# Kernel optimization log

Measured on AMD Instinct MI355X. Metric: run time of the kernel, lower is better.

The kernel has to match this reference:

```python
import jax, jax.numpy as jnp
import numpy as np

LN_EPS = 1e-5


def setup_inputs() -> dict:
    key = jax.random.key(0)
    kx, kA, kB, kC, kg = jax.random.split(key, 5)
    B, S, D, N = 16, 1024, 1024, 64
    x = jax.random.uniform(kx, (B, S, D), dtype=jnp.float32)
    A = jax.random.uniform(kA, (D, N), dtype=jnp.float32)          # torch.rand init
    W_B = jax.random.normal(kB, (N, D), dtype=jnp.float32) * 0.02  # B: d_model -> d_state
    W_C = jax.random.normal(kC, (D, N), dtype=jnp.float32) * 0.02  # C.weight_raw, [d_model, d_state]
    gamma = jax.random.normal(kg, (D,), dtype=jnp.float32) * 0.1   # TopologicalNorm scale (sigmoid-bounded)
    return {"x": x, "A": A, "W_B": W_B, "W_C": W_C, "gamma": gamma}


def reference(x, A, W_B, W_C, gamma):
    # x: [B, S, D]
    Bb, S, D = x.shape
    N = A.shape[1]
    A_sig = jax.nn.sigmoid(A)          # [D, N] state decay gates
    Bw = jax.nn.sigmoid(W_B)           # [N, D] sigmoid-constrained input projection
    Cw = jax.nn.sigmoid(W_C)           # [D, N] sigmoid-constrained readout weights
    g = jax.nn.sigmoid(gamma)          # [D]   bounded norm scale

    def step(h, x_t):
        # x_t: [B, D], h: [B, D, N]
        b_t = x_t @ Bw.T                                             # [B, N]
        inp = b_t[:, None, :] * x_t[:, :, None]                      # [B, D, N] outer product morphism
        h = jnp.clip(h * A_sig[None] + inp, 0.0, 1.0)                # clamped state update
        y = jnp.sum(h * Cw[None], axis=-1)                           # [B, D] weighted readout
        mu = jnp.mean(y, axis=-1, keepdims=True)
        var = jnp.var(y, axis=-1, keepdims=True)
        y = (y - mu) * jax.lax.rsqrt(var + LN_EPS) * g               # TopologicalNorm
        return h, y

    h0 = jnp.zeros((Bb, D, N), dtype=x.dtype)
    _, ys = jax.lax.scan(step, h0, jnp.swapaxes(x, 0, 1))            # ys: [S, B, D]
    y = jnp.swapaxes(ys, 0, 1)                                       # [B, S, D]
    return jnp.clip(y + x, 0.0, 1.0)
```

## Files before the change

kernel.cpp:

```cpp
#include <hip/hip_runtime.h>
#include <math.h>

#define D_MODEL 1024
#define N_STATE 64
#define BATCH   16
#define SEQ     1024
#define CS      16
#define SEGLEN  512
#define WARM    64
#define SAT_T   1.0001f
#define LPS     20

__device__ __forceinline__ float sigmoidf_dev(float v) {
    return 1.0f / (1.0f + expf(-v));
}

template<int CTRL>
__device__ __forceinline__ float dpp_add(float v) {
    int s = __builtin_amdgcn_update_dpp(0, __float_as_int(v), CTRL, 0xF, 0xF, true);
    return v + __int_as_float(s);
}

template<int CTRL>
__device__ __forceinline__ float dpp_min(float v) {
    int s = __builtin_amdgcn_update_dpp(0, __float_as_int(v), CTRL, 0xF, 0xF, true);
    return fminf(v, __int_as_float(s));
}

#define CLAMP01(v) __builtin_amdgcn_fmed3f((v), 0.0f, 1.0f)

__global__ __launch_bounds__(256) void k0_precompute(
        const float* __restrict__ A, const float* __restrict__ W_B,
        const float* __restrict__ W_C, const float* __restrict__ gamma,
        float* __restrict__ A_sig, float* __restrict__ BwT,
        float* __restrict__ Cs, float* __restrict__ gs) {
    int i = blockIdx.x * 256 + threadIdx.x;
    if (i < D_MODEL * N_STATE) {
        A_sig[i] = sigmoidf_dev(A[i]);
        Cs[i]    = sigmoidf_dev(W_C[i]);
        int d = i >> 6, n = i & 63;
        BwT[i] = sigmoidf_dev(W_B[n * D_MODEL + d]);
        if (i < D_MODEL) gs[i] = sigmoidf_dev(gamma[i]);
    }
}

__global__ __launch_bounds__(256) void k0b_csum(
        const float* __restrict__ Cs, float* __restrict__ csum) {
    int d = blockIdx.x * 256 + threadIdx.x;
    if (d >= D_MODEL) return;
    const float4* c = (const float4*)(Cs + (size_t)d * N_STATE);
    float w[16];
#pragma unroll
    for (int q = 0; q < 16; ++q) {
        float4 v = c[q];
        w[q] = (v.x + v.y) + (v.z + v.w);
    }
#pragma unroll
    for (int off = 1; off < 16; off <<= 1) {
        float tmp[16];
#pragma unroll
        for (int q = 0; q < 16; ++q) tmp[q] = w[q] + w[q ^ off];
#pragma unroll
        for (int q = 0; q < 16; ++q) w[q] = tmp[q];
    }
    csum[d] = w[0];
}

__global__ __launch_bounds__(256) void k1_bt_gemm(
        const float* __restrict__ x, const float* __restrict__ BwT,
        float* __restrict__ bt, float* __restrict__ btmin) {
    __shared__ float xs[2][32][17];
    __shared__ float bs[2][32][64];

    const int t  = threadIdx.x;
    const int r  = t >> 4;
    const int c  = t & 15;
    const int m0 = blockIdx.x * 16;

    const int xr = t >> 4;
    const int xk = (t & 15) * 2;

    float acc[4] = {0.f, 0.f, 0.f, 0.f};

    {
        float2 xv = *(const float2*)(x + (size_t)(m0 + xr) * D_MODEL + xk);
        float4 b0 = *(const float4*)(BwT + t * 4);
        float4 b1 = *(const float4*)(BwT + 1024 + t * 4);
        xs[0][xk + 0][xr] = xv.x;
        xs[0][xk + 1][xr] = xv.y;
        *(float4*)(&bs[0][0][0] + t * 4)        = b0;
        *(float4*)(&bs[0][0][0] + 1024 + t * 4) = b1;
    }
    __syncthreads();

    for (int kc = 0; kc < 32; ++kc) {
        const int p = kc & 1;
        float2 xv; float4 b0, b1;
        const bool more = (kc + 1 < 32);
        if (more) {
            const int k0 = (kc + 1) * 32;
            xv = *(const float2*)(x + (size_t)(m0 + xr) * D_MODEL + k0 + xk);
            b0 = *(const float4*)(BwT + (size_t)k0 * N_STATE + t * 4);
            b1 = *(const float4*)(BwT + (size_t)k0 * N_STATE + 1024 + t * 4);
        }
#pragma unroll
        for (int kk = 0; kk < 32; ++kk) {
            float  a  = xs[p][kk][r];
            float4 bq = *(const float4*)(&bs[p][kk][c * 4]);
            acc[0] = fmaf(a, bq.x, acc[0]);
            acc[1] = fmaf(a, bq.y, acc[1]);
            acc[2] = fmaf(a, bq.z, acc[2]);
            acc[3] = fmaf(a, bq.w, acc[3]);
        }
        if (more) {
            const int q = 1 - p;
            xs[q][xk + 0][xr] = xv.x;
            xs[q][xk + 1][xr] = xv.y;
            *(float4*)(&bs[q][0][0] + t * 4)        = b0;
            *(float4*)(&bs[q][0][0] + 1024 + t * 4) = b1;
        }
        __syncthreads();
    }

    *(float4*)(&bt[(size_t)(m0 + r) * N_STATE + c * 4]) =
        make_float4(acc[0], acc[1], acc[2], acc[3]);

    float bm = fminf(fminf(acc[0], acc[1]), fminf(acc[2], acc[3]));
    bm = dpp_min<0xB1>(bm); bm = dpp_min<0x4E>(bm);
    bm = dpp_min<0x141>(bm); bm = dpp_min<0x140>(bm);
    if (c == 0) btmin[m0 + r] = bm;
}

__global__ __launch_bounds__(256, 8) void k2_scan(
        const float* __restrict__ x, const float* __restrict__ bt,
        const float* __restrict__ btmin,
        const float* __restrict__ A_sig, const float* __restrict__ Cs,
        float* __restrict__ y_raw) {
    const int t    = threadIdx.x;
    const int lane = t & 63;
    const int wv   = t >> 6;
    const int nq   = lane & 15;
    const int cl   = wv * 4 + (lane >> 4);
    const int bid  = blockIdx.x;
    const int seg  = bid & 1;
    const int dg   = (bid >> 1) & 63;
    const int b    = bid >> 7;
    const int d0   = dg * 16;
    const int d    = d0 + cl;

    const int nWarm  = seg ? (WARM / CS) : 0;
    const int nTot   = nWarm + (SEGLEN / CS);
    const int sStart = seg * SEGLEN - nWarm * CS;

    __shared__ __align__(16) float lbt [2][CS * 64];
    __shared__ __align__(16) float lx  [2][CS * 16];
    __shared__ __align__(16) float lpxT[2][16 * LPS];

    const float4 av = *(const float4*)(A_sig + (size_t)d * N_STATE + nq * 4);
    const float4 cv = *(const float4*)(Cs    + (size_t)d * N_STATE + nq * 4);

    float h0 = 0.f, h1 = 0.f, h2 = 0.f, h3 = 0.f;

    const float* btp  = bt    + (size_t)b * SEQ * N_STATE + (size_t)sStart * N_STATE;
    const float* btmp = btmin + (size_t)b * SEQ + sStart;
    const float* xpp  = x + (size_t)b * SEQ * D_MODEL + (size_t)sStart * D_MODEL + d0;
    float* ystore = y_raw + (size_t)b * SEQ * D_MODEL + (size_t)seg * SEGLEN * D_MODEL + d;

    const int xst = t >> 4;
    const int xdd = t & 15;

    {
        float4 b4 = *(const float4*)(btp + t * 4);
        float  xv = xpp[(size_t)xst * D_MODEL + xdd];
        float  bm = fmaxf(btmp[xst], 0.f);
        *(float4*)(&lbt[0][t * 4]) = b4;
        lx[0][t] = xv;
        lpxT[0][xdd * LPS + xst] = xv * bm;
    }
    btp  += CS * N_STATE;
    btmp += CS;
    xpp  += (size_t)CS * D_MODEL;
    __syncthreads();

    for (int ch = 0; ch < nTot; ++ch) {
        const int p = ch & 1;
        float4 nb; float nx, npx;
        const bool more = (ch + 1 < nTot);
        if (more) {
            nb  = *(const float4*)(btp + t * 4);
            nx  = xpp[(size_t)xst * D_MODEL + xdd];
            npx = nx * fmaxf(btmp[xst], 0.f);
            btp  += CS * N_STATE;
            btmp += CS;
            xpp  += (size_t)CS * D_MODEL;
        }

        const float* Lb = lbt[p];
        const float* Lx = lx [p];
        const float* Lp = &lpxT[p][cl * LPS];

        if (ch < nWarm) {
#pragma unroll
            for (int g = 0; g < 4; ++g) {
                const float4 pq = *(const float4*)(Lp + g * 4);
                const float qmin = fminf(fminf(pq.x, pq.y), fminf(pq.z, pq.w));
                if (__all(qmin >= SAT_T)) { h0 = h1 = h2 = h3 = 1.f; continue; }
                const float pmv[4] = {pq.x, pq.y, pq.z, pq.w};
#pragma unroll
                for (int j = 0; j < 4; ++j) {
                    const int i = g * 4 + j;
                    const float pm = pmv[j];
                    if (__all(pm >= SAT_T)) { h0 = h1 = h2 = h3 = 1.f; continue; }
                    const float  xt = Lx[i * 16 + cl];
                    const float4 bv = *(const float4*)(Lb + i * 64 + nq * 4);
                    h0 = CLAMP01(fmaf(h0, av.x, bv.x * xt));
                    h1 = CLAMP01(fmaf(h1, av.y, bv.y * xt));
                    h2 = CLAMP01(fmaf(h2, av.z, bv.z * xt));
                    h3 = CLAMP01(fmaf(h3, av.w, bv.w * xt));
                }
            }
        } else {
#pragma unroll
            for (int g = 0; g < 4; ++g) {
                const float4 pq = *(const float4*)(Lp + g * 4);
                const float qmin = fminf(fminf(pq.x, pq.y), fminf(pq.z, pq.w));
                if (__all(qmin >= SAT_T)) { h0 = h1 = h2 = h3 = 1.f; continue; }
                const float pmv[4] = {pq.x, pq.y, pq.z, pq.w};
#pragma unroll
                for (int j = 0; j < 4; ++j) {
                    const int i = g * 4 + j;
                    const float pm = pmv[j];
                    if (__all(pm >= SAT_T)) { h0 = h1 = h2 = h3 = 1.f; continue; }
                    const float  xt = Lx[i * 16 + cl];
                    const float4 bv = *(const float4*)(Lb + i * 64 + nq * 4);
                    h0 = CLAMP01(fmaf(h0, av.x, bv.x * xt));
                    h1 = CLAMP01(fmaf(h1, av.y, bv.y * xt));
                    h2 = CLAMP01(fmaf(h2, av.z, bv.z * xt));
                    h3 = CLAMP01(fmaf(h3, av.w, bv.w * xt));
                    float y = fmaf(h0, cv.x, h1 * cv.y) + fmaf(h2, cv.z, h3 * cv.w);
                    y = dpp_add<0xB1>(y);
                    y = dpp_add<0x4E>(y);
                    y = dpp_add<0x141>(y);
                    y = dpp_add<0x140>(y);
                    if (nq == 0 && !(pm >= SAT_T)) ystore[(size_t)i * D_MODEL] = y;
                }
            }
            ystore += (size_t)CS * D_MODEL;
        }

        if (more) {
            const int q = 1 - p;
            *(float4*)(&lbt[q][t * 4]) = nb;
            lx[q][t] = nx;
            lpxT[q][xdd * LPS + xst] = npx;
        }
        __syncthreads();
    }
}

__global__ __launch_bounds__(256, 1) void k3_norm(
        const float* __restrict__ x, const float* __restrict__ gs,
        const float* __restrict__ btmin, const float* __restrict__ csum,
        float* __restrict__ y) {
    const int row = blockIdx.x;
    const int t   = threadIdx.x;
    const size_t base = (size_t)row * D_MODEL + t * 4;
    const float bm = fmaxf(btmin[row], 0.f);

    float4 xv  = *(const float4*)(x + base);
    float4 cs4 = *(const float4*)(csum + t * 4);
    const bool p0 = (xv.x * bm >= SAT_T);
    const bool p1 = (xv.y * bm >= SAT_T);
    const bool p2 = (xv.z * bm >= SAT_T);
    const bool p3 = (xv.w * bm >= SAT_T);
    float y0 = cs4.x, y1 = cs4.y, y2 = cs4.z, y3 = cs4.w;
    if (!(p0 && p1 && p2 && p3)) {
        float4 ld = *(const float4*)(y + base);
        if (!p0) y0 = ld.x;
        if (!p1) y1 = ld.y;
        if (!p2) y2 = ld.z;
        if (!p3) y3 = ld.w;
    }

    float s1 = (y0 + y1) + (y2 + y3);
#pragma unroll
    for (int off = 32; off > 0; off >>= 1) s1 += __shfl_xor(s1, off);

    __shared__ float red[8];
    const int w = t >> 6;
    if ((t & 63) == 0) red[w] = s1;
    __syncthreads();
    const float mu = (red[0] + red[1] + red[2] + red[3]) * (1.0f / (float)D_MODEL);

    const float dx0 = y0 - mu, dx1 = y1 - mu, dx2 = y2 - mu, dx3 = y3 - mu;
    float s2 = (dx0 * dx0 + dx1 * dx1) + (dx2 * dx2 + dx3 * dx3);
#pragma unroll
    for (int off = 32; off > 0; off >>= 1) s2 += __shfl_xor(s2, off);
    if ((t & 63) == 0) red[4 + w] = s2;
    __syncthreads();
    const float var = (red[4] + red[5] + red[6] + red[7]) * (1.0f / (float)D_MODEL);
    const float rs  = 1.0f / sqrtf(var + 1e-5f);

    float4 gv = *(const float4*)(gs + t * 4);
    float4 o;
    o.x = fminf(fmaxf(dx0 * rs * gv.x + xv.x, 0.f), 1.f);
    o.y = fminf(fmaxf(dx1 * rs * gv.y + xv.y, 0.f), 1.f);
    o.z = fminf(fmaxf(dx2 * rs * gv.z + xv.z, 0.f), 1.f);
    o.w = fminf(fmaxf(dx3 * rs * gv.w + xv.w, 0.f), 1.f);
    *(float4*)(y + base) = o;
}

extern "C" void kernel_launch(void* const* d_in, const int* in_sizes, int n_in,
                              void* d_out, int out_size, void* d_ws, size_t ws_size,
                              hipStream_t stream) {
    (void)in_sizes; (void)n_in; (void)out_size; (void)ws_size;
    const float* x     = (const float*)d_in[0];
    const float* A     = (const float*)d_in[1];
    const float* W_B   = (const float*)d_in[2];
    const float* W_C   = (const float*)d_in[3];
    const float* gamma = (const float*)d_in[4];
    float* out = (float*)d_out;
    float* ws  = (float*)d_ws;

    float* bt    = ws;
    float* A_sig = ws + 1048576;
    float* BwT   = ws + 1048576 + 65536;
    float* Cs    = ws + 1048576 + 2 * 65536;
    float* gs    = ws + 1048576 + 3 * 65536;
    float* btmin = ws + 1048576 + 3 * 65536 + 1024;
    float* csum  = ws + 1048576 + 3 * 65536 + 1024 + 16384;

    k0_precompute<<<dim3(256), dim3(256), 0, stream>>>(A, W_B, W_C, gamma,
                                                       A_sig, BwT, Cs, gs);
    k0b_csum<<<dim3(4), dim3(256), 0, stream>>>(Cs, csum);
    k1_bt_gemm<<<dim3(1024), dim3(256), 0, stream>>>(x, BwT, bt, btmin);
    k2_scan<<<dim3(2048), dim3(256), 0, stream>>>(x, bt, btmin, A_sig, Cs, out);
    k3_norm<<<dim3(BATCH * SEQ), dim3(256), 0, stream>>>(x, gs, btmin, csum, out);
}
```

Measured before the change: 231.8 us.

## Retile bt GEMM to 32 rows per block, load B weights directly into registers

Measured after the change: 259.2 us. 1.12x slower.

```diff
diff --git a/kernel.cpp b/kernel.cpp
--- a/kernel.cpp
+++ b/kernel.cpp
@@ -69,66 +69,79 @@
 __global__ __launch_bounds__(256) void k1_bt_gemm(
         const float* __restrict__ x, const float* __restrict__ BwT,
         float* __restrict__ bt, float* __restrict__ btmin) {
-    __shared__ float xs[2][32][17];
-    __shared__ float bs[2][32][64];
+    __shared__ float xs[2][16][36];
 
     const int t  = threadIdx.x;
     const int r  = t >> 4;
     const int c  = t & 15;
-    const int m0 = blockIdx.x * 16;
-
-    const int xr = t >> 4;
-    const int xk = (t & 15) * 2;
-
-    float acc[4] = {0.f, 0.f, 0.f, 0.f};
+    const int m0 = blockIdx.x * 32;
+
+    const int sm = t >> 3;
+    const int sk = (t & 7) * 2;
+
+    float acc[2][4];
+#pragma unroll
+    for (int i = 0; i < 2; ++i)
+#pragma unroll
+        for (int j = 0; j < 4; ++j) acc[i][j] = 0.0f;
 
     {
-        float2 xv = *(const float2*)(x + (size_t)(m0 + xr) * D_MODEL + xk);
-        float4 b0 = *(const float4*)(BwT + t * 4);
-        float4 b1 = *(const float4*)(BwT + 1024 + t * 4);
-        xs[0][xk + 0][xr] = xv.x;
-        xs[0][xk + 1][xr] = xv.y;
-        *(float4*)(&bs[0][0][0] + t * 4)        = b0;
-        *(float4*)(&bs[0][0][0] + 1024 + t * 4) = b1;
+        float2 xv = *(const float2*)(x + (size_t)(m0 + sm) * D_MODEL + sk);
+        xs[0][sk + 0][sm] = xv.x;
+        xs[0][sk + 1][sm] = xv.y;
     }
     __syncthreads();
 
-    for (int kc = 0; kc < 32; ++kc) {
-        const int p = kc & 1;
-        float2 xv; float4 b0, b1;
-        const bool more = (kc + 1 < 32);
-        if (more) {
-            const int k0 = (kc + 1) * 32;
-            xv = *(const float2*)(x + (size_t)(m0 + xr) * D_MODEL + k0 + xk);
-            b0 = *(const float4*)(BwT + (size_t)k0 * N_STATE + t * 4);
-            b1 = *(const float4*)(BwT + (size_t)k0 * N_STATE + 1024 + t * 4);
-        }
-#pragma unroll
-        for (int kk = 0; kk < 32; ++kk) {
-            float  a  = xs[p][kk][r];
-            float4 bq = *(const float4*)(&bs[p][kk][c * 4]);
-            acc[0] = fmaf(a, bq.x, acc[0]);
-            acc[1] = fmaf(a, bq.y, acc[1]);
-            acc[2] = fmaf(a, bq.z, acc[2]);
-            acc[3] = fmaf(a, bq.w, acc[3]);
-        }
+    for (int kt = 0; kt < 64; ++kt) {
+        const int p = kt & 1;
+        const bool more = (kt + 1 < 64);
+
+        float4 breg[16];
+#pragma unroll
+        for (int kk = 0; kk < 16; ++kk)
+            breg[kk] = *(const float4*)(BwT + (size_t)(kt * 16 + kk) * N_STATE + c * 4);
+
+        float2 xv;
+        if (more)
+            xv = *(const float2*)(x + (size_t)(m0 + sm) * D_MODEL + (kt + 1) * 16 + sk);
+
+#pragma unroll
+        for (int kk = 0; kk < 16; ++kk) {
+            float2 ap = *(const float2*)(&xs[p][kk][r * 2]);
+            acc[0][0] = fmaf(ap.x, breg[kk].x, acc[0][0]);
+            acc[0][1] = fmaf(ap.x, breg[kk].y, acc[0][1]);
+            acc[0][2] = fmaf(ap.x, breg[kk].z, acc[0][2]);
+            acc[0][3] = fmaf(ap.x, breg[kk].w, acc[0][3]);
+            acc[1][0] = fmaf(ap.y, breg[kk].x, acc[1][0]);
+            acc[1][1] = fmaf(ap.y, breg[kk].y, acc[1][1]);
+            acc[1][2] = fmaf(ap.y, breg[kk].z, acc[1][2]);
+            acc[1][3] = fmaf(ap.y, breg[kk].w, acc[1][3]);
+        }
+
         if (more) {
             const int q = 1 - p;
-            xs[q][xk + 0][xr] = xv.x;
-            xs[q][xk + 1][xr] = xv.y;
-            *(float4*)(&bs[q][0][0] + t * 4)        = b0;
-            *(float4*)(&bs[q][0][0] + 1024 + t * 4) = b1;
+            xs[q][sk + 0][sm] = xv.x;
+            xs[q][sk + 1][sm] = xv.y;
         }
         __syncthreads();
     }
 
-    *(float4*)(&bt[(size_t)(m0 + r) * N_STATE + c * 4]) =
-        make_float4(acc[0], acc[1], acc[2], acc[3]);
-
-    float bm = fminf(fminf(acc[0], acc[1]), fminf(acc[2], acc[3]));
-    bm = dpp_min<0xB1>(bm); bm = dpp_min<0x4E>(bm);
-    bm = dpp_min<0x141>(bm); bm = dpp_min<0x140>(bm);
-    if (c == 0) btmin[m0 + r] = bm;
+#pragma unroll
+    for (int i = 0; i < 2; ++i) {
+        float4 o = make_float4(acc[i][0], acc[i][1], acc[i][2], acc[i][3]);
+        *(float4*)(&bt[(size_t)(m0 + r * 2 + i) * N_STATE + c * 4]) = o;
+    }
+
+    float bm0 = fminf(fminf(acc[0][0], acc[0][1]), fminf(acc[0][2], acc[0][3]));
+    float bm1 = fminf(fminf(acc[1][0], acc[1][1]), fminf(acc[1][2], acc[1][3]));
+    bm0 = dpp_min<0xB1>(bm0); bm0 = dpp_min<0x4E>(bm0);
+    bm0 = dpp_min<0x141>(bm0); bm0 = dpp_min<0x140>(bm0);
+    bm1 = dpp_min<0xB1>(bm1); bm1 = dpp_min<0x4E>(bm1);
+    bm1 = dpp_min<0x141>(bm1); bm1 = dpp_min<0x140>(bm1);
+    if (c == 0) {
+        btmin[m0 + r * 2]     = bm0;
+        btmin[m0 + r * 2 + 1] = bm1;
+    }
 }
 
 __global__ __launch_bounds__(256, 8) void k2_scan(
@@ -333,7 +346,7 @@
     k0_precompute<<<dim3(256), dim3(256), 0, stream>>>(A, W_B, W_C, gamma,
                                                        A_sig, BwT, Cs, gs);
     k0b_csum<<<dim3(4), dim3(256), 0, stream>>>(Cs, csum);
-    k1_bt_gemm<<<dim3(1024), dim3(256), 0, stream>>>(x, BwT, bt, btmin);
+    k1_bt_gemm<<<dim3(512), dim3(256), 0, stream>>>(x, BwT, bt, btmin);
     k2_scan<<<dim3(2048), dim3(256), 0, stream>>>(x, bt, btmin, A_sig, Cs, out);
     k3_norm<<<dim3(BATCH * SEQ), dim3(256), 0, stream>>>(x, gs, btmin, csum, out);
 }
```
